# Performance work log

Hardware: AMD Instinct MI355X
Metric: run time of the kernel (lower is better)

## Reference

```python
import jax, jax.numpy as jnp
import numpy as np


def _batch_pairwise_dist(x, y):
    # x: [B, Nx, D] (gts), y: [B, Ny, D] (preds) -> P: [B, Nx, Ny] squared L2
    rx = jnp.sum(x * x, axis=-1)  # [B, Nx]
    ry = jnp.sum(y * y, axis=-1)  # [B, Ny]
    zz = jnp.einsum('bnd,bmd->bnm', x, y)  # [B, Nx, Ny]
    return rx[:, :, None] + ry[:, None, :] - 2.0 * zz


def setup_inputs() -> dict:
    key = jax.random.key(0)
    k1, k2, k3 = jax.random.split(key, 3)
    B, Ngt, Npred, D = 4, 4096, 4096, 3
    preds = jax.random.normal(k1, (B, Npred, D), dtype=jnp.float32)
    gts = jax.random.normal(k2, (B, Ngt, D), dtype=jnp.float32)
    mask = jax.random.randint(k3, (B, Ngt), 0, 2).astype(jnp.bool_)
    return {"preds": preds, "gts": gts, "mask": mask}


def reference(preds, gts, mask):
    # P[b, i, j] = ||gts[b,i] - preds[b,j]||^2
    P = _batch_pairwise_dist(gts, preds)  # [B, Ngt, Npred]
    # Directional term 1: for each pred point, min over VALID gt points.
    P_masked = jnp.where(mask[:, :, None], P, jnp.inf)  # invalid gt rows -> +inf
    loss_1 = jnp.sum(jnp.min(P_masked, axis=1))
    # Directional term 2: for each VALID gt point, min over all pred points.
    mins_gt = jnp.min(P, axis=2)  # [B, Ngt]
    loss_2 = jnp.sum(jnp.where(mask, mins_gt, 0.0))
    return loss_1 + loss_2
```

## Files before the change

### kernel.cpp

```cpp
#include <hip/hip_runtime.h>

#define NBATCH 4
#define NPTS   4096
#define YCHUNK 512
#define XCHUNK 512
#define NYC    (NPTS / YCHUNK)
#define NXC    (NPTS / XCHUNK)
#define BIGF   1e30f

__global__ __launch_bounds__(256)
void chamfer_min_kernel(const float* __restrict__ preds,
                        const float* __restrict__ gts,
                        const int* __restrict__ mask,
                        float* __restrict__ partial,
                        float* __restrict__ out) {
    const int zc  = blockIdx.z;
    const int dir = zc >> 2;
    const int b   = zc & 3;
    const int tid = threadIdx.x;

    if ((zc | blockIdx.x | blockIdx.y | tid) == 0) out[0] = 0.0f;

    const float* X = (dir == 0 ? preds : gts) + (size_t)b * NPTS * 3;
    const float* Y = (dir == 0 ? gts : preds) + (size_t)b * NPTS * 3;

    __shared__ float4 sy[YCHUNK];
    const int cbase = blockIdx.y * YCHUNK;
    for (int t = tid; t < YCHUNK; t += 256) {
        const int j = cbase + t;
        const float y0 = Y[j * 3 + 0];
        const float y1 = Y[j * 3 + 1];
        const float y2 = Y[j * 3 + 2];
        float ry = y0 * y0 + y1 * y1 + y2 * y2;
        if (dir == 0 && mask[b * NPTS + j] == 0) ry = BIGF;
        sy[t] = make_float4(y0, y1, y2, ry);
    }
    __syncthreads();

    const int xA = blockIdx.x * XCHUNK + tid;
    const int xB = xA + 256;
    float a0 = X[xA * 3 + 0], a1 = X[xA * 3 + 1], a2 = X[xA * 3 + 2];
    float c0 = X[xB * 3 + 0], c1 = X[xB * 3 + 1], c2 = X[xB * 3 + 2];
    const float rxA = a0 * a0 + a1 * a1 + a2 * a2;
    const float rxB = c0 * c0 + c1 * c1 + c2 * c2;
    a0 *= -2.0f; a1 *= -2.0f; a2 *= -2.0f;
    c0 *= -2.0f; c1 *= -2.0f; c2 *= -2.0f;

    float mA0 = BIGF, mA1 = BIGF;
    float mB0 = BIGF, mB1 = BIGF;

    #pragma unroll 4
    for (int k = 0; k < YCHUNK; k += 4) {
        const float4 p0 = sy[k + 0];
        const float4 p1 = sy[k + 1];
        const float4 p2 = sy[k + 2];
        const float4 p3 = sy[k + 3];

        const float tA0 = fmaf(a0, p0.x, fmaf(a1, p0.y, fmaf(a2, p0.z, p0.w)));
        const float tA1 = fmaf(a0, p1.x, fmaf(a1, p1.y, fmaf(a2, p1.z, p1.w)));
        const float tA2 = fmaf(a0, p2.x, fmaf(a1, p2.y, fmaf(a2, p2.z, p2.w)));
        const float tA3 = fmaf(a0, p3.x, fmaf(a1, p3.y, fmaf(a2, p3.z, p3.w)));
        mA0 = fminf(mA0, fminf(tA0, tA1));
        mA1 = fminf(mA1, fminf(tA2, tA3));

        const float tB0 = fmaf(c0, p0.x, fmaf(c1, p0.y, fmaf(c2, p0.z, p0.w)));
        const float tB1 = fmaf(c0, p1.x, fmaf(c1, p1.y, fmaf(c2, p1.z, p1.w)));
        const float tB2 = fmaf(c0, p2.x, fmaf(c1, p2.y, fmaf(c2, p2.z, p2.w)));
        const float tB3 = fmaf(c0, p3.x, fmaf(c1, p3.y, fmaf(c2, p3.z, p3.w)));
        mB0 = fminf(mB0, fminf(tB0, tB1));
        mB1 = fminf(mB1, fminf(tB2, tB3));
    }

    const float dA = rxA + fminf(mA0, mA1);
    const float dB = rxB + fminf(mB0, mB1);

    float* prow = partial + ((size_t)(dir * NBATCH + b) * NYC + blockIdx.y) * NPTS;
    prow[blockIdx.x * XCHUNK + tid] = dA;
    prow[blockIdx.x * XCHUNK + tid + 256] = dB;
}

__global__ __launch_bounds__(256)
void chamfer_reduce_kernel(const float* __restrict__ partial,
                           const int* __restrict__ mask,
                           float* __restrict__ out) {
    const int gid = blockIdx.x * blockDim.x + threadIdx.x;
    const int dir = gid >> 14;
    const int rem = gid & 16383;
    const int b   = rem >> 12;
    const int x   = rem & 4095;

    const float* p = partial + ((size_t)(dir * NBATCH + b) * NYC) * NPTS + x;
    float m = p[0];
    #pragma unroll
    for (int c = 1; c < NYC; ++c) m = fminf(m, p[(size_t)c * NPTS]);

    float v = m;
    if (dir == 1 && mask[b * NPTS + x] == 0) v = 0.0f;

    #pragma unroll
    for (int off = 32; off > 0; off >>= 1)
        v += __shfl_down(v, off, 64);

    __shared__ float wsum[4];
    const int wave = threadIdx.x >> 6;
    if ((threadIdx.x & 63) == 0) wsum[wave] = v;
    __syncthreads();
    if (threadIdx.x == 0)
        atomicAdd(out, wsum[0] + wsum[1] + wsum[2] + wsum[3]);
}

extern "C" void kernel_launch(void* const* d_in, const int* in_sizes, int n_in,
                              void* d_out, int out_size, void* d_ws, size_t ws_size,
                              hipStream_t stream) {
    const float* preds = (const float*)d_in[0];
    const float* gts   = (const float*)d_in[1];
    const int*   mask  = (const int*)d_in[2];
    float* out = (float*)d_out;

    float* partial = (float*)d_ws;

    dim3 grid(NXC, NYC, 2 * NBATCH);
    chamfer_min_kernel<<<grid, 256, 0, stream>>>(preds, gts, mask, partial, out);

    chamfer_reduce_kernel<<<(2 * NBATCH * NPTS) / 256, 256, 0, stream>>>(
        partial, mask, out);
}
```

Measured before the change: 22.57 us.

## Register-block 8 x-points per thread with smaller y-chunks and split reduction

```diff
diff --git a/kernel.cpp b/kernel.cpp
--- a/kernel.cpp
+++ b/kernel.cpp
@@ -2,10 +2,11 @@
 
 #define NBATCH 4
 #define NPTS   4096
-#define YCHUNK 512
-#define XCHUNK 512
+#define XPT    8
+#define XCHUNK (256 * XPT)
+#define NXC    (NPTS / XCHUNK)
+#define YCHUNK 128
 #define NYC    (NPTS / YCHUNK)
-#define NXC    (NPTS / XCHUNK)
 #define BIGF   1e30f
 
 __global__ __launch_bounds__(256)
@@ -26,57 +27,50 @@
 
     __shared__ float4 sy[YCHUNK];
     const int cbase = blockIdx.y * YCHUNK;
-    for (int t = tid; t < YCHUNK; t += 256) {
-        const int j = cbase + t;
+    if (tid < YCHUNK) {
+        const int j = cbase + tid;
         const float y0 = Y[j * 3 + 0];
         const float y1 = Y[j * 3 + 1];
         const float y2 = Y[j * 3 + 2];
         float ry = y0 * y0 + y1 * y1 + y2 * y2;
         if (dir == 0 && mask[b * NPTS + j] == 0) ry = BIGF;
-        sy[t] = make_float4(y0, y1, y2, ry);
+        sy[tid] = make_float4(y0, y1, y2, ry);
     }
     __syncthreads();
 
-    const int xA = blockIdx.x * XCHUNK + tid;
-    const int xB = xA + 256;
-    float a0 = X[xA * 3 + 0], a1 = X[xA * 3 + 1], a2 = X[xA * 3 + 2];
-    float c0 = X[xB * 3 + 0], c1 = X[xB * 3 + 1], c2 = X[xB * 3 + 2];
-    const float rxA = a0 * a0 + a1 * a1 + a2 * a2;
-    const float rxB = c0 * c0 + c1 * c1 + c2 * c2;
-    a0 *= -2.0f; a1 *= -2.0f; a2 *= -2.0f;
-    c0 *= -2.0f; c1 *= -2.0f; c2 *= -2.0f;
+    float a0[XPT], a1[XPT], a2[XPT], rx[XPT], m[XPT];
+    const int xbase = blockIdx.x * XCHUNK + tid;
+    #pragma unroll
+    for (int i = 0; i < XPT; ++i) {
+        const int x = xbase + i * 256;
+        float v0 = X[x * 3 + 0], v1 = X[x * 3 + 1], v2 = X[x * 3 + 2];
+        rx[i] = v0 * v0 + v1 * v1 + v2 * v2;
+        a0[i] = -2.0f * v0; a1[i] = -2.0f * v1; a2[i] = -2.0f * v2;
+        m[i] = BIGF;
+    }
 
-    float mA0 = BIGF, mA1 = BIGF;
-    float mB0 = BIGF, mB1 = BIGF;
-
-    #pragma unroll 4
+    #pragma unroll 2
     for (int k = 0; k < YCHUNK; k += 4) {
         const float4 p0 = sy[k + 0];
         const float4 p1 = sy[k + 1];
         const float4 p2 = sy[k + 2];
         const float4 p3 = sy[k + 3];
-
-        const float tA0 = fmaf(a0, p0.x, fmaf(a1, p0.y, fmaf(a2, p0.z, p0.w)));
-        const float tA1 = fmaf(a0, p1.x, fmaf(a1, p1.y, fmaf(a2, p1.z, p1.w)));
-        const float tA2 = fmaf(a0, p2.x, fmaf(a1, p2.y, fmaf(a2, p2.z, p2.w)));
-        const float tA3 = fmaf(a0, p3.x, fmaf(a1, p3.y, fmaf(a2, p3.z, p3.w)));
-        mA0 = fminf(mA0, fminf(tA0, tA1));
-        mA1 = fminf(mA1, fminf(tA2, tA3));
-
-        const float tB0 = fmaf(c0, p0.x, fmaf(c1, p0.y, fmaf(c2, p0.z, p0.w)));
-        const float tB1 = fmaf(c0, p1.x, fmaf(c1, p1.y, fmaf(c2, p1.z, p1.w)));
-        const float tB2 = fmaf(c0, p2.x, fmaf(c1, p2.y, fmaf(c2, p2.z, p2.w)));
-        const float tB3 = fmaf(c0, p3.x, fmaf(c1, p3.y, fmaf(c2, p3.z, p3.w)));
-        mB0 = fminf(mB0, fminf(tB0, tB1));
-        mB1 = fminf(mB1, fminf(tB2, tB3));
+        #pragma unroll
+        for (int i = 0; i < XPT; ++i) {
+            const float t0 = fmaf(a0[i], p0.x, fmaf(a1[i], p0.y, fmaf(a2[i], p0.z, p0.w)));
+            const float t1 = fmaf(a0[i], p1.x, fmaf(a1[i], p1.y, fmaf(a2[i], p1.z, p1.w)));
+            const float t2 = fmaf(a0[i], p2.x, fmaf(a1[i], p2.y, fmaf(a2[i], p2.z, p2.w)));
+            const float t3 = fmaf(a0[i], p3.x, fmaf(a1[i], p3.y, fmaf(a2[i], p3.z, p3.w)));
+            m[i] = fminf(fminf(m[i], t0), t1);
+            m[i] = fminf(fminf(m[i], t2), t3);
+        }
     }
 
-    const float dA = rxA + fminf(mA0, mA1);
-    const float dB = rxB + fminf(mB0, mB1);
-
-    float* prow = partial + ((size_t)(dir * NBATCH + b) * NYC + blockIdx.y) * NPTS;
-    prow[blockIdx.x * XCHUNK + tid] = dA;
-    prow[blockIdx.x * XCHUNK + tid + 256] = dB;
+    float* prow = partial + ((size_t)(dir * NBATCH + b) * NYC + blockIdx.y) * NPTS
+                + blockIdx.x * XCHUNK + tid;
+    #pragma unroll
+    for (int i = 0; i < XPT; ++i)
+        prow[i * 256] = rx[i] + m[i];
 }
 
 __global__ __launch_bounds__(256)
@@ -84,18 +78,25 @@
                            const int* __restrict__ mask,
                            float* __restrict__ out) {
     const int gid = blockIdx.x * blockDim.x + threadIdx.x;
-    const int dir = gid >> 14;
-    const int rem = gid & 16383;
-    const int b   = rem >> 12;
-    const int x   = rem & 4095;
+    const int h   = gid & 1;
+    const int p   = gid >> 1;
+    const int dir = p >> 14;
+    const int b   = (p >> 12) & 3;
+    const int x   = p & 4095;
 
-    const float* p = partial + ((size_t)(dir * NBATCH + b) * NYC) * NPTS + x;
-    float m = p[0];
+    const float* base = partial + ((size_t)(dir * NBATCH + b) * NYC) * NPTS + x
+                      + (size_t)(h * 16) * NPTS;
+    float m = base[0];
     #pragma unroll
-    for (int c = 1; c < NYC; ++c) m = fminf(m, p[(size_t)c * NPTS]);
+    for (int c = 1; c < 16; ++c) m = fminf(m, base[(size_t)c * NPTS]);
 
-    float v = m;
-    if (dir == 1 && mask[b * NPTS + x] == 0) v = 0.0f;
+    m = fminf(m, __shfl_xor(m, 1, 64));
+
+    float v = 0.0f;
+    if (h == 0) {
+        v = m;
+        if (dir == 1 && mask[b * NPTS + x] == 0) v = 0.0f;
+    }
 
     #pragma unroll
     for (int off = 32; off > 0; off >>= 1)
@@ -122,6 +123,6 @@
     dim3 grid(NXC, NYC, 2 * NBATCH);
     chamfer_min_kernel<<<grid, 256, 0, stream>>>(preds, gts, mask, partial, out);
 
-    chamfer_reduce_kernel<<<(2 * NBATCH * NPTS) / 256, 256, 0, stream>>>(
+    chamfer_reduce_kernel<<<2 * (2 * NBATCH * NPTS) / 256, 256, 0, stream>>>(
         partial, mask, out);
 }
```

New measurement: 22.88 us. About the same (+1.4%).
